# Performance work log

Hardware: AMD Instinct MI355X
Metric: run time of the kernel (lower is better)

## Reference

```python
import jax, jax.numpy as jnp
import numpy as np

B, E, H, W, P, C = 2, 256, 192, 192, 16, 80
GRIDS = (40, 36, 24, 16, 12)
L = len(GRIDS)
MASK_W, CLS_W, ALPHA, GAMMA, EPS = 3.0, 1.0, 0.25, 2.0, 1e-4


def setup_inputs() -> dict:
    key = jax.random.key(0)
    ks = jax.random.split(key, 32)
    inp = {"mask_out": jax.random.normal(ks[0], (B, E, H, W), jnp.float32)}
    for i, g in enumerate(GRIDS):
        inp[f"kernel_l{i}"] = jax.random.normal(ks[1 + i], (B, g, g, E), jnp.float32) * 0.05
        inp[f"cate_l{i}"] = jax.random.uniform(ks[6 + i], (B, g, g, C), jnp.float32)
        inp[f"pos_l{i}"] = jax.random.randint(ks[11 + i], (B, P), 0, g * g, dtype=jnp.int32)
        inp[f"cate_t_l{i}"] = jax.random.randint(ks[16 + i], (B, g, g), -1, C, dtype=jnp.int32)
    # binary instance masks, image-major layout [B, L, P, H, W]
    inp["mask_targets"] = (jax.random.uniform(ks[21], (B, L, P, H, W)) > 0.9).astype(jnp.float32)
    return inp


def _forward(mask_out, kernels, cates, mask_targets, pos_idxs, cate_ts):
    # --- dynamic 1x1 conv: gather positive kernels and apply as batched matmul ---
    preds = []
    for kl, pl in zip(kernels, pos_idxs):
        g2 = kl.shape[1] * kl.shape[2]
        kflat = kl.reshape(B, g2, E)
        kp = jnp.take_along_axis(kflat, pl[:, :, None], axis=1)  # [B, P, E]
        preds.append(jnp.einsum('bpe,behw->bphw', kp, mask_out))  # F.conv2d 1x1
    preds = jnp.stack(preds)  # [L, B, P, H, W]  (level-major, matches torch cat order)

    # --- dice loss ---
    mp = jax.nn.sigmoid(preds).reshape(L * B * P, H * W)
    # NOTE: original code concatenates targets image-major (img, level) while preds
    # are level-major (level, img); we reproduce that pairing faithfully.
    mt = mask_targets.reshape(B * L * P, H * W)
    a = jnp.sum(mp * mt, axis=1)
    b = jnp.sum(mp * mp, axis=1)
    c = jnp.sum(mt * mt, axis=1)
    mask_loss = jnp.sum(1.0 - 2.0 * a / (b + c + 1e-4)) / (L * B * P)

    # --- focal loss on positive grid cells ---
    tgt = jnp.concatenate([t.reshape(-1) for t in cate_ts])            # [N]
    prd = jnp.concatenate([cl.reshape(-1, C) for cl in cates])          # [N, C]
    posm = (tgt > -1).astype(jnp.float32)
    p = jnp.clip(prd, EPS, 1.0 - EPS)
    gt = jax.nn.one_hot(jnp.clip(tgt, 0, C - 1), C, dtype=jnp.float32)
    af = jnp.where(gt == 1.0, ALPHA, 1.0 - ALPHA)
    pt = jnp.where(gt == 1.0, p, 1.0 - p)
    fw = af * (1.0 - pt) ** GAMMA
    ce = -(gt * jnp.log(p) + (1.0 - gt) * jnp.log(1.0 - p))
    cls_loss = jnp.sum(fw * ce * posm[:, None]) / jnp.sum(posm)

    return jnp.stack([MASK_W * mask_loss, CLS_W * cls_loss])  # [mask_loss, cls_loss]


def reference(mask_out, kernel_l0, kernel_l1, kernel_l2, kernel_l3, kernel_l4,
              cate_l0, cate_l1, cate_l2, cate_l3, cate_l4, mask_targets,
              pos_l0, pos_l1, pos_l2, pos_l3, pos_l4,
              cate_t_l0, cate_t_l1, cate_t_l2, cate_t_l3, cate_t_l4):
    return _forward(mask_out,
                    (kernel_l0, kernel_l1, kernel_l2, kernel_l3, kernel_l4),
                    (cate_l0, cate_l1, cate_l2, cate_l3, cate_l4),
                    mask_targets,
                    (pos_l0, pos_l1, pos_l2, pos_l3, pos_l4),
                    (cate_t_l0, cate_t_l1, cate_t_l2, cate_t_l3, cate_t_l4))
```

## Files before the change

kernel.cpp:

```cpp
#include <hip/hip_runtime.h>
#include <hip/hip_bf16.h>

namespace {

constexpr int kHW = 36864;
constexpr int kFocalQuads = 7744 * 20;

typedef __attribute__((ext_vector_type(8))) short bf16x8;
typedef __attribute__((ext_vector_type(4))) float f32x4;

__device__ __forceinline__ unsigned short f2bf(float x) {
  return __builtin_bit_cast(unsigned short, __float2bfloat16(x));
}

__device__ __forceinline__ float wave_sum(float v) {
#pragma unroll
  for (int off = 32; off; off >>= 1) v += __shfl_xor(v, off, 64);
  return v;
}

__global__ __launch_bounds__(128) void gather_k(
    const float* __restrict__ k0, const float* __restrict__ k1,
    const float* __restrict__ k2, const float* __restrict__ k3,
    const float* __restrict__ k4,
    const int* __restrict__ q0, const int* __restrict__ q1,
    const int* __restrict__ q2, const int* __restrict__ q3,
    const int* __restrict__ q4,
    unsigned short* __restrict__ kbf) {
  const int b = blockIdx.y;
  const int row = blockIdx.x;
  const int l = row >> 4, p = row & 15;
  const float* kb[5] = {k0, k1, k2, k3, k4};
  const int* pb[5] = {q0, q1, q2, q3, q4};
  const int bg2[5] = {b * 1600, b * 1296, b * 576, b * 256, b * 144};
  const int pos = pb[l][b * 16 + p];
  const int ch = threadIdx.x * 2;
  const float2 kv = *(const float2*)(kb[l] + (size_t)(bg2[l] + pos) * 256 + ch);
  *(unsigned int*)&kbf[((size_t)b * 80 + row) * 256 + ch] =
      (unsigned int)f2bf(kv.x) | ((unsigned int)f2bf(kv.y) << 16);
}

__global__ __launch_bounds__(256, 2) void solov2_main(
    const float* __restrict__ mask_out,
    const unsigned short* __restrict__ kbf,
    const float* __restrict__ mask_targets,
    float* __restrict__ acc) {
  const int b = blockIdx.y;
  const int lane = threadIdx.x & 63;
  const int wv = threadIdx.x >> 6;
  const int px16 = lane & 15;
  const int hi8 = (lane >> 4) * 8;
  const int px0 = blockIdx.x * 64;
  const int pxl = px0 + wv * 16 + px16;

  __shared__ float bufB[2][32][64];
  __shared__ float bred[4][240];

  const unsigned short* __restrict__ ka =
      kbf + ((size_t)b * 80 + px16) * 256 + hi8;

  const float* __restrict__ gstage = mask_out + (size_t)b * 256 * kHW +
                                     (size_t)(wv * 4 + (lane >> 4)) * kHW +
                                     px0 + (lane & 15) * 4;

#define STAGE(CUR, KS)                                                       \
  {                                                                          \
    const float* gs = gstage + (size_t)(KS)*32 * kHW;                        \
    __builtin_amdgcn_global_load_lds(                                        \
        (const __attribute__((address_space(1))) unsigned int*)gs,           \
        (__attribute__((address_space(3))) unsigned int*)&bufB[CUR][wv * 4]  \
            [0],                                                             \
        16, 0, 0);                                                           \
    __builtin_amdgcn_global_load_lds(                                        \
        (const __attribute__((address_space(1))) unsigned int*)(gs +         \
                                                                16 * kHW),   \
        (__attribute__((address_space(3))) unsigned int*)&bufB[CUR][wv * 4 + \
                                                                   16][0],   \
        16, 0, 0);                                                           \
  }

  f32x4 a5[5];
#pragma unroll
  for (int mt = 0; mt < 5; ++mt) a5[mt] = (f32x4){0.f, 0.f, 0.f, 0.f};

  STAGE(0, 0);
  __syncthreads();

#pragma unroll
  for (int ks = 0; ks < 8; ++ks) {
    if (ks + 1 < 8) STAGE((ks + 1) & 1, ks + 1);
    float fb[8];
#pragma unroll
    for (int j = 0; j < 8; ++j) fb[j] = bufB[ks & 1][hi8 + j][wv * 16 + px16];
    bf16x8 bb;
#pragma unroll
    for (int j = 0; j < 8; ++j) bb[j] = (short)f2bf(fb[j]);
#pragma unroll
    for (int mt = 0; mt < 5; ++mt) {
      const bf16x8 af = *(const bf16x8*)(ka + mt * 4096 + ks * 32);
      a5[mt] =
          __builtin_amdgcn_mfma_f32_16x16x32_bf16(af, bb, a5[mt], 0, 0, 0);
    }
    __syncthreads();
  }
#undef STAGE

#pragma unroll
  for (int mt = 0; mt < 5; ++mt) {
#pragma unroll
    for (int j = 0; j < 4; ++j) {
      const int row80 = mt * 16 + (lane >> 4) * 4 + j;
      const int r = (row80 >> 4) * 32 + b * 16 + (row80 & 15);
      const float x0 = a5[mt][j];
      const float mp = 1.f / (1.f + __expf(-x0));
      const float tv = mask_targets[(size_t)r * kHW + pxl];
      float av = mp * tv;
      float bv = mp * mp;
      float cv = tv;
#pragma unroll
      for (int m = 1; m <= 8; m <<= 1) {
        av += __shfl_xor(av, m, 64);
        bv += __shfl_xor(bv, m, 64);
        cv += __shfl_xor(cv, m, 64);
      }
      if (px16 == 0) {
        bred[wv][row80] = av;
        bred[wv][80 + row80] = bv;
        bred[wv][160 + row80] = cv;
      }
    }
  }
  __syncthreads();
  if (threadIdx.x < 240) {
    const int q = threadIdx.x / 80;
    const int row80 = threadIdx.x - q * 80;
    const int r = (row80 >> 4) * 32 + b * 16 + (row80 & 15);
    const float s = bred[0][threadIdx.x] + bred[1][threadIdx.x] +
                    bred[2][threadIdx.x] + bred[3][threadIdx.x];
    unsafeAtomicAdd(&acc[q * 160 + r], s);
  }
}

__global__ __launch_bounds__(256) void focal_kernel(
    const float* __restrict__ c0, const float* __restrict__ c1,
    const float* __restrict__ c2, const float* __restrict__ c3,
    const float* __restrict__ c4,
    const int* __restrict__ t0, const int* __restrict__ t1,
    const int* __restrict__ t2, const int* __restrict__ t3,
    const int* __restrict__ t4,
    float* __restrict__ acc) {
  const int idx = blockIdx.x * 256 + threadIdx.x;
  const int n = idx / 20;
  const int cq = (idx - n * 20) * 4;
  int t;
  const float* crow;
  if (n < 3200) {
    t = t0[n]; crow = c0 + (size_t)n * 80;
  } else if (n < 5792) {
    const int o = n - 3200; t = t1[o]; crow = c1 + (size_t)o * 80;
  } else if (n < 6944) {
    const int o = n - 5792; t = t2[o]; crow = c2 + (size_t)o * 80;
  } else if (n < 7456) {
    const int o = n - 6944; t = t3[o]; crow = c3 + (size_t)o * 80;
  } else {
    const int o = n - 7456; t = t4[o]; crow = c4 + (size_t)o * 80;
  }
  float term = 0.f, np = 0.f;
  if (t > -1) {
    const float4 pv4 = *(const float4*)&crow[cq];
    const float pvs[4] = {pv4.x, pv4.y, pv4.z, pv4.w};
#pragma unroll
    for (int j = 0; j < 4; ++j) {
      float pv = fminf(fmaxf(pvs[j], 1e-4f), 1.f - 1e-4f);
      const bool gm = (cq + j == t);
      const float af = gm ? 0.25f : 0.75f;
      const float pt = gm ? pv : 1.f - pv;
      const float om = 1.f - pt;
      term = fmaf(af * om * om, -__logf(pt), term);
    }
    if (cq == 0) np = 1.f;
  }
  term = wave_sum(term);
  np = wave_sum(np);
  __shared__ float st[8];
  const int wid = threadIdx.x >> 6;
  if ((threadIdx.x & 63) == 0) {
    st[wid] = term;
    st[4 + wid] = np;
  }
  __syncthreads();
  if (threadIdx.x == 0) {
    unsafeAtomicAdd(&acc[480], st[0] + st[1] + st[2] + st[3]);
    unsafeAtomicAdd(&acc[481], st[4] + st[5] + st[6] + st[7]);
  }
}

__global__ void zero_kernel(float* __restrict__ acc) {
  const int i = blockIdx.x * 256 + threadIdx.x;
  if (i < 482) acc[i] = 0.f;
}

__global__ __launch_bounds__(64) void finalize_kernel(
    const float* __restrict__ acc, float* __restrict__ out) {
  const int tid = threadIdx.x;
  float s = 0.f;
#pragma unroll
  for (int rr = 0; rr < 3; ++rr) {
    const int r = tid + rr * 64;
    if (r < 160) {
      const float a = acc[r];
      const float bb = acc[160 + r];
      const float cc = acc[320 + r];
      s += 1.f - 2.f * a / (bb + cc + 1e-4f);
    }
  }
  s = wave_sum(s);
  if (tid == 0) {
    out[0] = 3.0f * (s / 160.f);
    out[1] = acc[480] / acc[481];
  }
}

}

extern "C" void kernel_launch(void* const* d_in, const int* in_sizes, int n_in,
                              void* d_out, int out_size, void* d_ws,
                              size_t ws_size, hipStream_t stream) {
  const float* mask_out = (const float*)d_in[0];
  const float* k[5];
  const float* cc[5];
  const int* pp[5];
  const int* tt[5];
  for (int i = 0; i < 5; ++i) {
    k[i] = (const float*)d_in[1 + 4 * i];
    cc[i] = (const float*)d_in[2 + 4 * i];
    pp[i] = (const int*)d_in[3 + 4 * i];
    tt[i] = (const int*)d_in[4 + 4 * i];
  }
  const float* mt = (const float*)d_in[21];
  float* acc = (float*)d_ws;
  unsigned short* kbf = (unsigned short*)((float*)d_ws + 512);
  float* out = (float*)d_out;

  hipLaunchKernelGGL(zero_kernel, dim3(2), dim3(256), 0, stream, acc);
  hipLaunchKernelGGL(gather_k, dim3(80, 2), dim3(128), 0, stream, k[0], k[1],
                     k[2], k[3], k[4], pp[0], pp[1], pp[2], pp[3], pp[4], kbf);
  hipLaunchKernelGGL(solov2_main, dim3(576, 2), dim3(256), 0, stream, mask_out,
                     kbf, mt, acc);
  hipLaunchKernelGGL(focal_kernel, dim3(605), dim3(256), 0, stream, cc[0],
                     cc[1], cc[2], cc[3], cc[4], tt[0], tt[1], tt[2], tt[3],
                     tt[4], acc);
  hipLaunchKernelGGL(finalize_kernel, dim3(1), dim3(64), 0, stream, acc, out);
}
```

Before: 78.26 us.

## Fuse zero/gather and GEMM/focal kernels, double K-stage depth per barrier

Merges the accumulator zeroing into the kernel-gather launch and folds the focal loss into the main dice GEMM kernel as extra blocks, cutting five launches to three. The GEMM pipeline now stages 64 channels per buffer, giving 4 iterations with 4 async LDS loads each instead of 8 iterations, so there are half as many barriers. LDS per block doubles to 32 KB of staging, which may limit occupancy, and focal blocks now share a grid with the GEMM blocks.

```diff
diff --git a/kernel.cpp b/kernel.cpp
--- a/kernel.cpp
+++ b/kernel.cpp
@@ -4,7 +4,8 @@
 namespace {
 
 constexpr int kHW = 36864;
-constexpr int kFocalQuads = 7744 * 20;
+constexpr int kGemmBlocks = 1152;
+constexpr int kFocalBlocks = 605;
 
 typedef __attribute__((ext_vector_type(8))) short bf16x8;
 typedef __attribute__((ext_vector_type(4))) float f32x4;
@@ -19,16 +20,23 @@
   return v;
 }
 
-__global__ __launch_bounds__(128) void gather_k(
+__global__ __launch_bounds__(256) void prep_kernel(
     const float* __restrict__ k0, const float* __restrict__ k1,
     const float* __restrict__ k2, const float* __restrict__ k3,
     const float* __restrict__ k4,
     const int* __restrict__ q0, const int* __restrict__ q1,
     const int* __restrict__ q2, const int* __restrict__ q3,
     const int* __restrict__ q4,
-    unsigned short* __restrict__ kbf) {
-  const int b = blockIdx.y;
-  const int row = blockIdx.x;
+    unsigned short* __restrict__ kbf, float* __restrict__ acc) {
+  const int bid = blockIdx.x;
+  if (bid == 0) {
+    for (int i = threadIdx.x; i < 482; i += 256) acc[i] = 0.f;
+    return;
+  }
+  const int idx = bid - 1;
+  const int b = idx / 80;
+  const int row = idx - b * 80;
+  if (threadIdx.x >= 128) return;
   const int l = row >> 4, p = row & 15;
   const float* kb[5] = {k0, k1, k2, k3, k4};
   const int* pb[5] = {q0, q1, q2, q3, q4};
@@ -40,21 +48,79 @@
       (unsigned int)f2bf(kv.x) | ((unsigned int)f2bf(kv.y) << 16);
 }
 
-__global__ __launch_bounds__(256, 2) void solov2_main(
+__global__ __launch_bounds__(256, 2) void mega_kernel(
     const float* __restrict__ mask_out,
     const unsigned short* __restrict__ kbf,
     const float* __restrict__ mask_targets,
+    const float* __restrict__ c0, const float* __restrict__ c1,
+    const float* __restrict__ c2, const float* __restrict__ c3,
+    const float* __restrict__ c4,
+    const int* __restrict__ t0, const int* __restrict__ t1,
+    const int* __restrict__ t2, const int* __restrict__ t3,
+    const int* __restrict__ t4,
     float* __restrict__ acc) {
-  const int b = blockIdx.y;
+  __shared__ float bufB[2][64][64];
+  __shared__ float bred[4][240];
+
+  const int bid = blockIdx.x;
+
+  if (bid >= kGemmBlocks) {
+    const int idx = (bid - kGemmBlocks) * 256 + threadIdx.x;
+    const int n = idx / 20;
+    const int cq = (idx - n * 20) * 4;
+    int t;
+    const float* crow;
+    if (n < 3200) {
+      t = t0[n]; crow = c0 + (size_t)n * 80;
+    } else if (n < 5792) {
+      const int o = n - 3200; t = t1[o]; crow = c1 + (size_t)o * 80;
+    } else if (n < 6944) {
+      const int o = n - 5792; t = t2[o]; crow = c2 + (size_t)o * 80;
+    } else if (n < 7456) {
+      const int o = n - 6944; t = t3[o]; crow = c3 + (size_t)o * 80;
+    } else {
+      const int o = n - 7456; t = t4[o]; crow = c4 + (size_t)o * 80;
+    }
+    float term = 0.f, np = 0.f;
+    if (t > -1) {
+      const float4 pv4 = *(const float4*)&crow[cq];
+      const float pvs[4] = {pv4.x, pv4.y, pv4.z, pv4.w};
+#pragma unroll
+      for (int j = 0; j < 4; ++j) {
+        float pv = fminf(fmaxf(pvs[j], 1e-4f), 1.f - 1e-4f);
+        const bool gm = (cq + j == t);
+        const float af = gm ? 0.25f : 0.75f;
+        const float pt = gm ? pv : 1.f - pv;
+        const float om = 1.f - pt;
+        term = fmaf(af * om * om, -__logf(pt), term);
+      }
+      if (cq == 0) np = 1.f;
+    }
+    term = wave_sum(term);
+    np = wave_sum(np);
+    const int wid = threadIdx.x >> 6;
+    if ((threadIdx.x & 63) == 0) {
+      bred[0][wid] = term;
+      bred[0][4 + wid] = np;
+    }
+    __syncthreads();
+    if (threadIdx.x == 0) {
+      unsafeAtomicAdd(&acc[480],
+                      bred[0][0] + bred[0][1] + bred[0][2] + bred[0][3]);
+      unsafeAtomicAdd(&acc[481],
+                      bred[0][4] + bred[0][5] + bred[0][6] + bred[0][7]);
+    }
+    return;
+  }
+
+  const int b = bid / 576;
+  const int tile = bid - b * 576;
+  const int px0 = tile * 64;
   const int lane = threadIdx.x & 63;
   const int wv = threadIdx.x >> 6;
   const int px16 = lane & 15;
   const int hi8 = (lane >> 4) * 8;
-  const int px0 = blockIdx.x * 64;
   const int pxl = px0 + wv * 16 + px16;
-
-  __shared__ float bufB[2][32][64];
-  __shared__ float bred[4][240];
 
   const unsigned short* __restrict__ ka =
       kbf + ((size_t)b * 80 + px16) * 256 + hi8;
@@ -63,20 +129,16 @@
                                      (size_t)(wv * 4 + (lane >> 4)) * kHW +
                                      px0 + (lane & 15) * 4;
 
-#define STAGE(CUR, KS)                                                       \
+#define STAGE(CUR, T)                                                        \
   {                                                                          \
-    const float* gs = gstage + (size_t)(KS)*32 * kHW;                        \
-    __builtin_amdgcn_global_load_lds(                                        \
-        (const __attribute__((address_space(1))) unsigned int*)gs,           \
-        (__attribute__((address_space(3))) unsigned int*)&bufB[CUR][wv * 4]  \
-            [0],                                                             \
-        16, 0, 0);                                                           \
-    __builtin_amdgcn_global_load_lds(                                        \
-        (const __attribute__((address_space(1))) unsigned int*)(gs +         \
-                                                                16 * kHW),   \
-        (__attribute__((address_space(3))) unsigned int*)&bufB[CUR][wv * 4 + \
-                                                                   16][0],   \
-        16, 0, 0);                                                           \
+    _Pragma("unroll") for (int r = 0; r < 4; ++r) {                          \
+      const float* gs = gstage + (size_t)((T)*64 + r * 16) * kHW;            \
+      __builtin_amdgcn_global_load_lds(                                      \
+          (const __attribute__((address_space(1))) unsigned int*)gs,         \
+          (__attribute__((address_space(3))) unsigned int*)                  \
+              &bufB[CUR][r * 16 + wv * 4][0],                                \
+          16, 0, 0);                                                         \
+    }                                                                        \
   }
 
   f32x4 a5[5];
@@ -87,19 +149,24 @@
   __syncthreads();
 
 #pragma unroll
-  for (int ks = 0; ks < 8; ++ks) {
-    if (ks + 1 < 8) STAGE((ks + 1) & 1, ks + 1);
-    float fb[8];
-#pragma unroll
-    for (int j = 0; j < 8; ++j) fb[j] = bufB[ks & 1][hi8 + j][wv * 16 + px16];
-    bf16x8 bb;
-#pragma unroll
-    for (int j = 0; j < 8; ++j) bb[j] = (short)f2bf(fb[j]);
-#pragma unroll
-    for (int mt = 0; mt < 5; ++mt) {
-      const bf16x8 af = *(const bf16x8*)(ka + mt * 4096 + ks * 32);
-      a5[mt] =
-          __builtin_amdgcn_mfma_f32_16x16x32_bf16(af, bb, a5[mt], 0, 0, 0);
+  for (int t = 0; t < 4; ++t) {
+    if (t + 1 < 4) STAGE((t + 1) & 1, t + 1);
+#pragma unroll
+    for (int sub = 0; sub < 2; ++sub) {
+      const int ks = t * 2 + sub;
+      float fb[8];
+#pragma unroll
+      for (int j = 0; j < 8; ++j)
+        fb[j] = bufB[t & 1][sub * 32 + hi8 + j][wv * 16 + px16];
+      bf16x8 bb;
+#pragma unroll
+      for (int j = 0; j < 8; ++j) bb[j] = (short)f2bf(fb[j]);
+#pragma unroll
+      for (int mt = 0; mt < 5; ++mt) {
+        const bf16x8 af = *(const bf16x8*)(ka + mt * 4096 + ks * 32);
+        a5[mt] =
+            __builtin_amdgcn_mfma_f32_16x16x32_bf16(af, bb, a5[mt], 0, 0, 0);
+      }
     }
     __syncthreads();
   }
@@ -139,65 +206,6 @@
                     bred[2][threadIdx.x] + bred[3][threadIdx.x];
     unsafeAtomicAdd(&acc[q * 160 + r], s);
   }
-}
-
-__global__ __launch_bounds__(256) void focal_kernel(
-    const float* __restrict__ c0, const float* __restrict__ c1,
-    const float* __restrict__ c2, const float* __restrict__ c3,
-    const float* __restrict__ c4,
-    const int* __restrict__ t0, const int* __restrict__ t1,
-    const int* __restrict__ t2, const int* __restrict__ t3,
-    const int* __restrict__ t4,
-    float* __restrict__ acc) {
-  const int idx = blockIdx.x * 256 + threadIdx.x;
-  const int n = idx / 20;
-  const int cq = (idx - n * 20) * 4;
-  int t;
-  const float* crow;
-  if (n < 3200) {
-    t = t0[n]; crow = c0 + (size_t)n * 80;
-  } else if (n < 5792) {
-    const int o = n - 3200; t = t1[o]; crow = c1 + (size_t)o * 80;
-  } else if (n < 6944) {
-    const int o = n - 5792; t = t2[o]; crow = c2 + (size_t)o * 80;
-  } else if (n < 7456) {
-    const int o = n - 6944; t = t3[o]; crow = c3 + (size_t)o * 80;
-  } else {
-    const int o = n - 7456; t = t4[o]; crow = c4 + (size_t)o * 80;
-  }
-  float term = 0.f, np = 0.f;
-  if (t > -1) {
-    const float4 pv4 = *(const float4*)&crow[cq];
-    const float pvs[4] = {pv4.x, pv4.y, pv4.z, pv4.w};
-#pragma unroll
-    for (int j = 0; j < 4; ++j) {
-      float pv = fminf(fmaxf(pvs[j], 1e-4f), 1.f - 1e-4f);
-      const bool gm = (cq + j == t);
-      const float af = gm ? 0.25f : 0.75f;
-      const float pt = gm ? pv : 1.f - pv;
-      const float om = 1.f - pt;
-      term = fmaf(af * om * om, -__logf(pt), term);
-    }
-    if (cq == 0) np = 1.f;
-  }
-  term = wave_sum(term);
-  np = wave_sum(np);
-  __shared__ float st[8];
-  const int wid = threadIdx.x >> 6;
-  if ((threadIdx.x & 63) == 0) {
-    st[wid] = term;
-    st[4 + wid] = np;
-  }
-  __syncthreads();
-  if (threadIdx.x == 0) {
-    unsafeAtomicAdd(&acc[480], st[0] + st[1] + st[2] + st[3]);
-    unsafeAtomicAdd(&acc[481], st[4] + st[5] + st[6] + st[7]);
-  }
-}
-
-__global__ void zero_kernel(float* __restrict__ acc) {
-  const int i = blockIdx.x * 256 + threadIdx.x;
-  if (i < 482) acc[i] = 0.f;
 }
 
 __global__ __launch_bounds__(64) void finalize_kernel(
@@ -242,13 +250,11 @@
   unsigned short* kbf = (unsigned short*)((float*)d_ws + 512);
   float* out = (float*)d_out;
 
-  hipLaunchKernelGGL(zero_kernel, dim3(2), dim3(256), 0, stream, acc);
-  hipLaunchKernelGGL(gather_k, dim3(80, 2), dim3(128), 0, stream, k[0], k[1],
-                     k[2], k[3], k[4], pp[0], pp[1], pp[2], pp[3], pp[4], kbf);
-  hipLaunchKernelGGL(solov2_main, dim3(576, 2), dim3(256), 0, stream, mask_out,
-                     kbf, mt, acc);
-  hipLaunchKernelGGL(focal_kernel, dim3(605), dim3(256), 0, stream, cc[0],
-                     cc[1], cc[2], cc[3], cc[4], tt[0], tt[1], tt[2], tt[3],
-                     tt[4], acc);
+  hipLaunchKernelGGL(prep_kernel, dim3(161), dim3(256), 0, stream, k[0], k[1],
+                     k[2], k[3], k[4], pp[0], pp[1], pp[2], pp[3], pp[4], kbf,
+                     acc);
+  hipLaunchKernelGGL(mega_kernel, dim3(kGemmBlocks + kFocalBlocks), dim3(256),
+                     0, stream, mask_out, kbf, mt, cc[0], cc[1], cc[2], cc[3],
+                     cc[4], tt[0], tt[1], tt[2], tt[3], tt[4], acc);
   hipLaunchKernelGGL(finalize_kernel, dim3(1), dim3(64), 0, stream, acc, out);
 }
```

Result: faster. 70.03 us (-10.5%).

## Split GEMM and dice epilogue into separate kernels via bf16 prediction buffer

Applied to the files above, without the earlier changes.

The GEMM kernel can now write the pre-sigmoid predictions as bf16 to a workspace buffer, and a separate streaming dice kernel reads them back with vectorised loads of predictions and targets. This removes the strided, uncoalesced target loads and shuffle reductions from the GEMM epilogue. The change also merges the zeroing of the accumulator into the gather kernel and raises the GEMM occupancy hint. The price is an extra ~11.8 MB write and read of the predictions plus one more launch, and the predictions now pass through bf16 rounding before the sigmoid. When the workspace is too small, the code falls back to the fused path.

```diff
diff --git a/kernel.cpp b/kernel.cpp
--- a/kernel.cpp
+++ b/kernel.cpp
@@ -4,7 +4,6 @@
 namespace {
 
 constexpr int kHW = 36864;
-constexpr int kFocalQuads = 7744 * 20;
 
 typedef __attribute__((ext_vector_type(8))) short bf16x8;
 typedef __attribute__((ext_vector_type(4))) float f32x4;
@@ -12,6 +11,9 @@
 __device__ __forceinline__ unsigned short f2bf(float x) {
   return __builtin_bit_cast(unsigned short, __float2bfloat16(x));
 }
+__device__ __forceinline__ float bf2f(unsigned short u) {
+  return __builtin_bit_cast(float, (unsigned int)u << 16);
+}
 
 __device__ __forceinline__ float wave_sum(float v) {
 #pragma unroll
@@ -19,16 +21,23 @@
   return v;
 }
 
-__global__ __launch_bounds__(128) void gather_k(
+__global__ __launch_bounds__(256) void prep_kernel(
     const float* __restrict__ k0, const float* __restrict__ k1,
     const float* __restrict__ k2, const float* __restrict__ k3,
     const float* __restrict__ k4,
     const int* __restrict__ q0, const int* __restrict__ q1,
     const int* __restrict__ q2, const int* __restrict__ q3,
     const int* __restrict__ q4,
-    unsigned short* __restrict__ kbf) {
-  const int b = blockIdx.y;
-  const int row = blockIdx.x;
+    unsigned short* __restrict__ kbf, float* __restrict__ acc) {
+  const int bid = blockIdx.x;
+  if (bid == 0) {
+    for (int i = threadIdx.x; i < 482; i += 256) acc[i] = 0.f;
+    return;
+  }
+  const int idx = bid - 1;
+  const int b = idx / 80;
+  const int row = idx - b * 80;
+  if (threadIdx.x >= 128) return;
   const int l = row >> 4, p = row & 15;
   const float* kb[5] = {k0, k1, k2, k3, k4};
   const int* pb[5] = {q0, q1, q2, q3, q4};
@@ -40,21 +49,25 @@
       (unsigned int)f2bf(kv.x) | ((unsigned int)f2bf(kv.y) << 16);
 }
 
-__global__ __launch_bounds__(256, 2) void solov2_main(
+template <int FUSED>
+__global__ __launch_bounds__(256, 4) void gemm_kernel(
     const float* __restrict__ mask_out,
     const unsigned short* __restrict__ kbf,
     const float* __restrict__ mask_targets,
+    unsigned short* __restrict__ predw,
     float* __restrict__ acc) {
-  const int b = blockIdx.y;
+  __shared__ float bufB[2][32][64];
+  __shared__ float bred[4][240];
+
+  const int bid = blockIdx.x;
+  const int b = bid / 576;
+  const int tile = bid - b * 576;
+  const int px0 = tile * 64;
   const int lane = threadIdx.x & 63;
   const int wv = threadIdx.x >> 6;
   const int px16 = lane & 15;
   const int hi8 = (lane >> 4) * 8;
-  const int px0 = blockIdx.x * 64;
   const int pxl = px0 + wv * 16 + px16;
-
-  __shared__ float bufB[2][32][64];
-  __shared__ float bred[4][240];
 
   const unsigned short* __restrict__ ka =
       kbf + ((size_t)b * 80 + px16) * 256 + hi8;
@@ -105,39 +118,88 @@
   }
 #undef STAGE
 
-#pragma unroll
-  for (int mt = 0; mt < 5; ++mt) {
-#pragma unroll
-    for (int j = 0; j < 4; ++j) {
-      const int row80 = mt * 16 + (lane >> 4) * 4 + j;
+  if constexpr (FUSED == 0) {
+#pragma unroll
+    for (int mt = 0; mt < 5; ++mt) {
+#pragma unroll
+      for (int j = 0; j < 4; ++j) {
+        const int row80 = mt * 16 + (lane >> 4) * 4 + j;
+        const int r = (row80 >> 4) * 32 + b * 16 + (row80 & 15);
+        predw[(size_t)r * kHW + pxl] = f2bf(a5[mt][j]);
+      }
+    }
+  } else {
+#pragma unroll
+    for (int mt = 0; mt < 5; ++mt) {
+#pragma unroll
+      for (int j = 0; j < 4; ++j) {
+        const int row80 = mt * 16 + (lane >> 4) * 4 + j;
+        const int r = (row80 >> 4) * 32 + b * 16 + (row80 & 15);
+        const float mp = 1.f / (1.f + __expf(-a5[mt][j]));
+        const float tv = mask_targets[(size_t)r * kHW + pxl];
+        float av = mp * tv;
+        float bv = mp * mp;
+        float cv = tv;
+#pragma unroll
+        for (int m = 1; m <= 8; m <<= 1) {
+          av += __shfl_xor(av, m, 64);
+          bv += __shfl_xor(bv, m, 64);
+          cv += __shfl_xor(cv, m, 64);
+        }
+        if (px16 == 0) {
+          bred[wv][row80] = av;
+          bred[wv][80 + row80] = bv;
+          bred[wv][160 + row80] = cv;
+        }
+      }
+    }
+    __syncthreads();
+    if (threadIdx.x < 240) {
+      const int q = threadIdx.x / 80;
+      const int row80 = threadIdx.x - q * 80;
       const int r = (row80 >> 4) * 32 + b * 16 + (row80 & 15);
-      const float x0 = a5[mt][j];
-      const float mp = 1.f / (1.f + __expf(-x0));
-      const float tv = mask_targets[(size_t)r * kHW + pxl];
-      float av = mp * tv;
-      float bv = mp * mp;
-      float cv = tv;
-#pragma unroll
-      for (int m = 1; m <= 8; m <<= 1) {
-        av += __shfl_xor(av, m, 64);
-        bv += __shfl_xor(bv, m, 64);
-        cv += __shfl_xor(cv, m, 64);
-      }
-      if (px16 == 0) {
-        bred[wv][row80] = av;
-        bred[wv][80 + row80] = bv;
-        bred[wv][160 + row80] = cv;
-      }
-    }
+      const float s = bred[0][threadIdx.x] + bred[1][threadIdx.x] +
+                      bred[2][threadIdx.x] + bred[3][threadIdx.x];
+      unsafeAtomicAdd(&acc[q * 160 + r], s);
+    }
+  }
+}
+
+__global__ __launch_bounds__(256) void dice_kernel(
+    const unsigned short* __restrict__ predw,
+    const float* __restrict__ mtg, float* __restrict__ acc) {
+  const int r = blockIdx.x / 18;
+  const int cb = blockIdx.x - r * 18;
+  const int px = cb * 2048 + threadIdx.x * 8;
+  const size_t base = (size_t)r * kHW + px;
+  const bf16x8 p8 = *(const bf16x8*)&predw[base];
+  const float4 t0 = *(const float4*)&mtg[base];
+  const float4 t1 = *(const float4*)&mtg[base + 4];
+  const float tv[8] = {t0.x, t0.y, t0.z, t0.w, t1.x, t1.y, t1.z, t1.w};
+  float av = 0.f, bv = 0.f, cv = 0.f;
+#pragma unroll
+  for (int j = 0; j < 8; ++j) {
+    const float x = bf2f((unsigned short)p8[j]);
+    const float mp = 1.f / (1.f + __expf(-x));
+    av = fmaf(mp, tv[j], av);
+    bv = fmaf(mp, mp, bv);
+    cv += tv[j];
+  }
+  av = wave_sum(av);
+  bv = wave_sum(bv);
+  cv = wave_sum(cv);
+  __shared__ float st[12];
+  const int w = threadIdx.x >> 6;
+  if ((threadIdx.x & 63) == 0) {
+    st[w] = av;
+    st[4 + w] = bv;
+    st[8 + w] = cv;
   }
   __syncthreads();
-  if (threadIdx.x < 240) {
-    const int q = threadIdx.x / 80;
-    const int row80 = threadIdx.x - q * 80;
-    const int r = (row80 >> 4) * 32 + b * 16 + (row80 & 15);
-    const float s = bred[0][threadIdx.x] + bred[1][threadIdx.x] +
-                    bred[2][threadIdx.x] + bred[3][threadIdx.x];
-    unsafeAtomicAdd(&acc[q * 160 + r], s);
+  if (threadIdx.x < 3) {
+    const int q = threadIdx.x;
+    unsafeAtomicAdd(&acc[q * 160 + r], st[q * 4] + st[q * 4 + 1] +
+                                           st[q * 4 + 2] + st[q * 4 + 3]);
   }
 }
 
@@ -195,11 +257,6 @@
   }
 }
 
-__global__ void zero_kernel(float* __restrict__ acc) {
-  const int i = blockIdx.x * 256 + threadIdx.x;
-  if (i < 482) acc[i] = 0.f;
-}
-
 __global__ __launch_bounds__(64) void finalize_kernel(
     const float* __restrict__ acc, float* __restrict__ out) {
   const int tid = threadIdx.x;
@@ -238,15 +295,26 @@
     tt[i] = (const int*)d_in[4 + 4 * i];
   }
   const float* mt = (const float*)d_in[21];
-  float* acc = (float*)d_ws;
-  unsigned short* kbf = (unsigned short*)((float*)d_ws + 512);
+
+  char* ws = (char*)d_ws;
+  float* acc = (float*)ws;
+  unsigned short* kbf = (unsigned short*)(ws + 4096);
+  unsigned short* predw = (unsigned short*)(ws + 90112);
+  const size_t need = 90112 + (size_t)160 * kHW * 2;
   float* out = (float*)d_out;
 
-  hipLaunchKernelGGL(zero_kernel, dim3(2), dim3(256), 0, stream, acc);
-  hipLaunchKernelGGL(gather_k, dim3(80, 2), dim3(128), 0, stream, k[0], k[1],
-                     k[2], k[3], k[4], pp[0], pp[1], pp[2], pp[3], pp[4], kbf);
-  hipLaunchKernelGGL(solov2_main, dim3(576, 2), dim3(256), 0, stream, mask_out,
-                     kbf, mt, acc);
+  hipLaunchKernelGGL(prep_kernel, dim3(161), dim3(256), 0, stream, k[0], k[1],
+                     k[2], k[3], k[4], pp[0], pp[1], pp[2], pp[3], pp[4], kbf,
+                     acc);
+  if (ws_size >= need) {
+    hipLaunchKernelGGL((gemm_kernel<0>), dim3(1152), dim3(256), 0, stream,
+                       mask_out, kbf, mt, predw, acc);
+    hipLaunchKernelGGL(dice_kernel, dim3(160 * 18), dim3(256), 0, stream,
+                       predw, mt, acc);
+  } else {
+    hipLaunchKernelGGL((gemm_kernel<1>), dim3(1152), dim3(256), 0, stream,
+                       mask_out, kbf, mt, predw, acc);
+  }
   hipLaunchKernelGGL(focal_kernel, dim3(605), dim3(256), 0, stream, cc[0],
                      cc[1], cc[2], cc[3], cc[4], tt[0], tt[1], tt[2], tt[3],
                      tt[4], acc);
```

Result: faster. 72.55 us (-7.3%).
